# Kernel tuning notes

Measured on AMD Instinct MI355X. Metric: run time of the kernel, lower is better.

## Reference

```python
import jax, jax.numpy as jnp
import numpy as np

B, S, C = 128, 4096, 64


def setup_inputs() -> dict:
    key = jax.random.key(0)
    k1, k2 = jax.random.split(key)
    logits = jax.random.normal(k1, (B, S, C), dtype=jnp.float32)
    prior_knowledge_matrix = jax.random.normal(k2, (C, C), dtype=jnp.float32)
    return {"logits": logits, "prior_knowledge_matrix": prior_knowledge_matrix}


def reference(logits, prior_knowledge_matrix):
    # log_softmax over class dim
    p = jax.nn.log_softmax(logits, axis=-1)  # [B, S, C]
    # per adjacent pair: diag(p_i @ M @ p_{i+1}^T) over the batch dim,
    # fused across all seq steps: 'bic,cd,bid->bi'
    loss_matrix = jnp.einsum("bic,cd,bid->bi", p[:, :-1, :], prior_knowledge_matrix, p[:, 1:, :])
    return loss_matrix  # [B, S-1]
```

## Files before the change

kernel.cpp:

```cpp
#include <hip/hip_runtime.h>
#include <hip/hip_bf16.h>

#define SS 4096
#define CC 64
#define PST 72
#define ROWS 129

typedef __attribute__((ext_vector_type(8))) short short8;
typedef __attribute__((ext_vector_type(4))) float floatx4;

static __device__ __forceinline__ unsigned short f2bf(float f) {
    __hip_bfloat16 h = __float2bfloat16(f);
    return *reinterpret_cast<unsigned short*>(&h);
}

__global__ __launch_bounds__(256, 4) void pkl_kernel(
        const float* __restrict__ logits,
        const float* __restrict__ M,
        float* __restrict__ out) {
    __shared__ __hip_bfloat16 m_lds[CC * PST];
    __shared__ __hip_bfloat16 p_lds[ROWS * PST];

    const int tid  = threadIdx.x;
    const int lane = tid & 63;
    const int w    = tid >> 6;
    const int quad = lane >> 4;
    const int nlo  = lane & 15;

    const int b  = blockIdx.x >> 5;
    const int s0 = (blockIdx.x & 31) * 128;

    for (int j = 0; j < 16; ++j) {
        int idx = j * 256 + tid;
        m_lds[(idx >> 6) * PST + (idx & 63)] = __float2bfloat16(M[idx]);
    }

    const float LOG2E = 1.4426950408889634f, LN2 = 0.6931471805599453f;
    for (int j = 0; j < 9; ++j) {
        int lr = j * 16 + w * 4 + quad;
        if (lr <= 128) {
            int grow = s0 + lr; if (grow > SS - 1) grow = SS - 1;
            const float4 x = *reinterpret_cast<const float4*>(
                logits + ((size_t)b * SS + grow) * CC + nlo * 4);
            float mx = fmaxf(fmaxf(x.x, x.y), fmaxf(x.z, x.w));
            #pragma unroll
            for (int o = 8; o > 0; o >>= 1) mx = fmaxf(mx, __shfl_xor(mx, o));
            float sm = exp2f((x.x - mx) * LOG2E) + exp2f((x.y - mx) * LOG2E)
                     + exp2f((x.z - mx) * LOG2E) + exp2f((x.w - mx) * LOG2E);
            #pragma unroll
            for (int o = 8; o > 0; o >>= 1) sm += __shfl_xor(sm, o);
            float lse = mx + log2f(sm) * LN2;
            ushort4 pk;
            pk.x = f2bf(x.x - lse); pk.y = f2bf(x.y - lse);
            pk.z = f2bf(x.z - lse); pk.w = f2bf(x.w - lse);
            *reinterpret_cast<ushort4*>(
                reinterpret_cast<unsigned short*>(p_lds) + lr * PST + nlo * 4) = pk;
        }
    }
    __syncthreads();

    floatx4 acc[2][4];
    #pragma unroll
    for (int mt = 0; mt < 2; ++mt)
        #pragma unroll
        for (int nt = 0; nt < 4; ++nt)
            acc[mt][nt] = (floatx4){0.f, 0.f, 0.f, 0.f};

    #pragma unroll
    for (int kt = 0; kt < 2; ++kt) {
        const int koff = kt * 32 + quad * 8;
        short8 bfrag[4];
        #pragma unroll
        for (int nt = 0; nt < 4; ++nt)
            bfrag[nt] = *reinterpret_cast<const short8*>(
                reinterpret_cast<const short*>(m_lds) + (nt * 16 + nlo) * PST + koff);
        #pragma unroll
        for (int mt = 0; mt < 2; ++mt) {
            short8 afrag = *reinterpret_cast<const short8*>(
                reinterpret_cast<const short*>(p_lds) + (w * 32 + 1 + mt * 16 + nlo) * PST + koff);
            #pragma unroll
            for (int nt = 0; nt < 4; ++nt)
                acc[mt][nt] = __builtin_amdgcn_mfma_f32_16x16x32_bf16(
                    afrag, bfrag[nt], acc[mt][nt], 0, 0, 0);
        }
    }

    const size_t outbase = (size_t)b * (SS - 1);
    #pragma unroll
    for (int mt = 0; mt < 2; ++mt)
        #pragma unroll
        for (int r = 0; r < 4; ++r) {
            const int lrow = w * 32 + mt * 16 + quad * 4 + r;
            float s = 0.f;
            #pragma unroll
            for (int nt = 0; nt < 4; ++nt)
                s += __bfloat162float(p_lds[lrow * PST + nt * 16 + nlo]) * acc[mt][nt][r];
            #pragma unroll
            for (int o = 8; o > 0; o >>= 1) s += __shfl_xor(s, o);
            if (nlo == 0) {
                int t = s0 + lrow;
                if (t <= SS - 2) out[outbase + t] = s;
            }
        }
}

extern "C" void kernel_launch(void* const* d_in, const int* in_sizes, int n_in,
                              void* d_out, int out_size, void* d_ws, size_t ws_size,
                              hipStream_t stream) {
    const float* logits = (const float*)d_in[0];
    const float* M      = (const float*)d_in[1];
    float* out          = (float*)d_out;

    dim3 grid(128 * 32), block(256);
    hipLaunchKernelGGL(pkl_kernel, grid, block, 0, stream, logits, M, out);
}
```

Before: 196.2 us.

## Permute class layout in LDS and use DPP reductions for softmax and dot

Each thread now loads four float4s per row, with four lanes covering a row, and computes the log-softmax over 16 values in registers. The row max and sum are reduced across the four lanes with DPP instead of a 16-lane shuffle reduction. The class dimension is stored permuted in LDS, and M's columns get the same permutation, so the epilogue can read four contiguous bf16 values with one ushort4 load and reduce with DPP row ops. This is meant to cut shuffle and LDS instruction overhead, at the cost of more register use and fewer lanes cooperating on each row, which lowers memory-level parallelism per load.

Result: faster. 188.8 us (-3.8%).

```diff
diff --git a/kernel.cpp b/kernel.cpp
--- a/kernel.cpp
+++ b/kernel.cpp
@@ -4,7 +4,7 @@
 #define SS 4096
 #define CC 64
 #define PST 72
-#define ROWS 129
+#define NROWS 129
 
 typedef __attribute__((ext_vector_type(8))) short short8;
 typedef __attribute__((ext_vector_type(4))) float floatx4;
@@ -12,50 +12,136 @@
 static __device__ __forceinline__ unsigned short f2bf(float f) {
     __hip_bfloat16 h = __float2bfloat16(f);
     return *reinterpret_cast<unsigned short*>(&h);
+}
+static __device__ __forceinline__ float bf2f(unsigned short u) {
+    __hip_bfloat16 h; *reinterpret_cast<unsigned short*>(&h) = u;
+    return __bfloat162float(h);
+}
+static __device__ __forceinline__ float f4c(const float4& v, int k) {
+    switch (k & 3) { case 0: return v.x; case 1: return v.y; case 2: return v.z; default: return v.w; }
+}
+
+#define DPP_QX1 0xB1
+#define DPP_QX2 0x4E
+#define DPP_HM  0x141
+#define DPP_RM  0x140
+template<int CTRL>
+static __device__ __forceinline__ float dpp_fadd(float v) {
+    int p = __builtin_amdgcn_update_dpp(0, __float_as_int(v), CTRL, 0xf, 0xf, true);
+    return v + __int_as_float(p);
+}
+template<int CTRL>
+static __device__ __forceinline__ float dpp_fmax(float v) {
+    int p = __builtin_amdgcn_update_dpp(0, __float_as_int(v), CTRL, 0xf, 0xf, true);
+    return fmaxf(v, __int_as_float(p));
 }
 
 __global__ __launch_bounds__(256, 4) void pkl_kernel(
         const float* __restrict__ logits,
         const float* __restrict__ M,
         float* __restrict__ out) {
-    __shared__ __hip_bfloat16 m_lds[CC * PST];
-    __shared__ __hip_bfloat16 p_lds[ROWS * PST];
+    __shared__ __hip_bfloat16 mt_lds[CC * PST];
+    __shared__ __hip_bfloat16 pt_lds[NROWS * PST];
 
     const int tid  = threadIdx.x;
     const int lane = tid & 63;
     const int w    = tid >> 6;
     const int quad = lane >> 4;
     const int nlo  = lane & 15;
+    const int rq   = lane >> 2;
+    const int q    = lane & 3;
 
     const int b  = blockIdx.x >> 5;
     const int s0 = (blockIdx.x & 31) * 128;
-
-    for (int j = 0; j < 16; ++j) {
-        int idx = j * 256 + tid;
-        m_lds[(idx >> 6) * PST + (idx & 63)] = __float2bfloat16(M[idx]);
-    }
-
+    const float* lg = logits + (size_t)b * SS * CC;
     const float LOG2E = 1.4426950408889634f, LN2 = 0.6931471805599453f;
-    for (int j = 0; j < 9; ++j) {
-        int lr = j * 16 + w * 4 + quad;
-        if (lr <= 128) {
-            int grow = s0 + lr; if (grow > SS - 1) grow = SS - 1;
-            const float4 x = *reinterpret_cast<const float4*>(
-                logits + ((size_t)b * SS + grow) * CC + nlo * 4);
-            float mx = fmaxf(fmaxf(x.x, x.y), fmaxf(x.z, x.w));
-            #pragma unroll
-            for (int o = 8; o > 0; o >>= 1) mx = fmaxf(mx, __shfl_xor(mx, o));
-            float sm = exp2f((x.x - mx) * LOG2E) + exp2f((x.y - mx) * LOG2E)
-                     + exp2f((x.z - mx) * LOG2E) + exp2f((x.w - mx) * LOG2E);
-            #pragma unroll
-            for (int o = 8; o > 0; o >>= 1) sm += __shfl_xor(sm, o);
-            float lse = mx + log2f(sm) * LN2;
-            ushort4 pk;
-            pk.x = f2bf(x.x - lse); pk.y = f2bf(x.y - lse);
-            pk.z = f2bf(x.z - lse); pk.w = f2bf(x.w - lse);
-            *reinterpret_cast<ushort4*>(
-                reinterpret_cast<unsigned short*>(p_lds) + lr * PST + nlo * 4) = pk;
-        }
+
+    float4 xa[2][4];
+    #pragma unroll
+    for (int i = 0; i < 2; ++i) {
+        const int lr = i * 64 + w * 16 + rq;
+        const float* rp = lg + (size_t)(s0 + lr) * CC;
+        #pragma unroll
+        for (int j = 0; j < 4; ++j)
+            xa[i][j] = *reinterpret_cast<const float4*>(rp + (j * 4 + q) * 4);
+    }
+
+    const int mc = tid >> 2;
+    float mv[16];
+    #pragma unroll
+    for (int k = 0; k < 4; ++k)
+        #pragma unroll
+        for (int j = 0; j < 4; ++j)
+            mv[4 * k + j] = M[mc * CC + 16 * j + 4 * q + k];
+    {
+        short8 g0, g1;
+        #pragma unroll
+        for (int o = 0; o < 8; ++o) { g0[o] = (short)f2bf(mv[o]); g1[o] = (short)f2bf(mv[o + 8]); }
+        short* mp = reinterpret_cast<short*>(mt_lds) + mc * PST + 16 * q;
+        *reinterpret_cast<short8*>(mp) = g0;
+        *reinterpret_cast<short8*>(mp + 8) = g1;
+    }
+
+    #pragma unroll
+    for (int i = 0; i < 2; ++i) {
+        const int lr = i * 64 + w * 16 + rq;
+        float mx = f4c(xa[i][0], 0);
+        #pragma unroll
+        for (int j = 0; j < 4; ++j)
+            #pragma unroll
+            for (int k = 0; k < 4; ++k)
+                mx = fmaxf(mx, f4c(xa[i][j], k));
+        mx = dpp_fmax<DPP_QX1>(mx); mx = dpp_fmax<DPP_QX2>(mx);
+        float sm = 0.f;
+        #pragma unroll
+        for (int j = 0; j < 4; ++j)
+            #pragma unroll
+            for (int k = 0; k < 4; ++k)
+                sm += exp2f((f4c(xa[i][j], k) - mx) * LOG2E);
+        sm = dpp_fadd<DPP_QX1>(sm); sm = dpp_fadd<DPP_QX2>(sm);
+        const float lse = mx + log2f(sm) * LN2;
+        short8 h0, h1;
+        #pragma unroll
+        for (int o = 0; o < 8; ++o) {
+            h0[o] = (short)f2bf(f4c(xa[i][o & 3], o >> 2) - lse);
+            h1[o] = (short)f2bf(f4c(xa[i][(o + 8) & 3], (o + 8) >> 2) - lse);
+        }
+        short* pp = reinterpret_cast<short*>(pt_lds) + lr * PST + 16 * q;
+        *reinterpret_cast<short8*>(pp) = h0;
+        *reinterpret_cast<short8*>(pp + 8) = h1;
+    }
+
+    if (tid < 4) {
+        const int grow = min(s0 + 128, SS - 1);
+        const float* rp = lg + (size_t)grow * CC;
+        float4 y[4];
+        #pragma unroll
+        for (int j = 0; j < 4; ++j)
+            y[j] = *reinterpret_cast<const float4*>(rp + (j * 4 + tid) * 4);
+        float mx = f4c(y[0], 0);
+        #pragma unroll
+        for (int j = 0; j < 4; ++j)
+            #pragma unroll
+            for (int k = 0; k < 4; ++k)
+                mx = fmaxf(mx, f4c(y[j], k));
+        mx = dpp_fmax<DPP_QX1>(mx); mx = dpp_fmax<DPP_QX2>(mx);
+        float sm = 0.f;
+        #pragma unroll
+        for (int j = 0; j < 4; ++j)
+            #pragma unroll
+            for (int k = 0; k < 4; ++k)
+                sm += exp2f((f4c(y[j], k) - mx) * LOG2E);
+        sm = dpp_fadd<DPP_QX1>(sm); sm = dpp_fadd<DPP_QX2>(sm);
+        const float lse = mx + log2f(sm) * LN2;
+        short8 h0, h1;
+        #pragma unroll
+        for (int o = 0; o < 8; ++o) {
+            h0[o] = (short)f2bf(f4c(y[o & 3], o >> 2) - lse);
+            h1[o] = (short)f2bf(f4c(y[(o + 8) & 3], (o + 8) >> 2) - lse);
+        }
+        short* pp = reinterpret_cast<short*>(pt_lds) + 128 * PST + 16 * tid;
+        *reinterpret_cast<short8*>(pp) = h0;
+        *reinterpret_cast<short8*>(pp + 8) = h1;
     }
     __syncthreads();
 
@@ -73,11 +159,11 @@
         #pragma unroll
         for (int nt = 0; nt < 4; ++nt)
             bfrag[nt] = *reinterpret_cast<const short8*>(
-                reinterpret_cast<const short*>(m_lds) + (nt * 16 + nlo) * PST + koff);
+                reinterpret_cast<const short*>(mt_lds) + (nt * 16 + nlo) * PST + koff);
         #pragma unroll
         for (int mt = 0; mt < 2; ++mt) {
             short8 afrag = *reinterpret_cast<const short8*>(
-                reinterpret_cast<const short*>(p_lds) + (w * 32 + 1 + mt * 16 + nlo) * PST + koff);
+                reinterpret_cast<const short*>(pt_lds) + (w * 32 + 1 + mt * 16 + nlo) * PST + koff);
             #pragma unroll
             for (int nt = 0; nt < 4; ++nt)
                 acc[mt][nt] = __builtin_amdgcn_mfma_f32_16x16x32_bf16(
@@ -91,14 +177,14 @@
         #pragma unroll
         for (int r = 0; r < 4; ++r) {
             const int lrow = w * 32 + mt * 16 + quad * 4 + r;
-            float s = 0.f;
-            #pragma unroll
-            for (int nt = 0; nt < 4; ++nt)
-                s += __bfloat162float(p_lds[lrow * PST + nt * 16 + nlo]) * acc[mt][nt][r];
-            #pragma unroll
-            for (int o = 8; o > 0; o >>= 1) s += __shfl_xor(s, o);
+            ushort4 pd = *reinterpret_cast<const ushort4*>(
+                reinterpret_cast<const unsigned short*>(pt_lds) + lrow * PST + 4 * nlo);
+            float s = bf2f(pd.x) * acc[mt][0][r] + bf2f(pd.y) * acc[mt][1][r]
+                    + bf2f(pd.z) * acc[mt][2][r] + bf2f(pd.w) * acc[mt][3][r];
+            s = dpp_fadd<DPP_QX1>(s); s = dpp_fadd<DPP_QX2>(s);
+            s = dpp_fadd<DPP_HM>(s);  s = dpp_fadd<DPP_RM>(s);
             if (nlo == 0) {
-                int t = s0 + lrow;
+                const int t = s0 + lrow;
                 if (t <= SS - 2) out[outbase + t] = s;
             }
         }
```
